# Performance work log

Hardware: AMD Instinct MI355X
Metric: run time of the kernel (lower is better)

## Reference

```python
import jax, jax.numpy as jnp
import numpy as np


def setup_inputs() -> dict:
    key = jax.random.key(0)
    ks = jax.random.split(key, 6)
    B, L, C = 32, 336, 512
    t = L // 2 + 1  # 169 rfft frequencies; four_l must equal t
    s = 1.0 / np.sqrt(C)
    return {
        "x": jax.random.normal(ks[0], (B, L, C), jnp.float32),
        "Wr": jax.random.normal(ks[1], (t, C, C), jnp.float32) * s,  # real part of complex Linear weights [t, out, in]
        "Wi": jax.random.normal(ks[2], (t, C, C), jnp.float32) * s,  # imag part
        "br": jax.random.normal(ks[3], (t, C), jnp.float32) * s,
        "bi": jax.random.normal(ks[4], (t, C), jnp.float32) * s,
        "weights": jax.random.normal(ks[5], (t,), jnp.float32),
    }


def reference(x, Wr, Wi, br, bi, weights):
    # x: [B, L, C] real. rfft along time with ortho norm -> [B, t, C] complex.
    B, L, C = x.shape
    t = Wr.shape[0]
    n = 2 * (t - 1)  # torch irfft default output length (== L, L even)
    xf = jnp.fft.rfft(x, axis=1, norm='ortho')  # [B, t, C] complex64

    # Per-frequency complex linear: y[b,i,o] = sum_c xf[b,i,c] * W[i,o,c] + b[i,o].
    # This fuses the original repeat + eye-mask + python loop into one batched GEMM.
    W = Wr + 1j * Wi
    b = br + 1j * bi
    y = jnp.einsum('bic,ioc->bio', xf, W) + b[None]  # [B, t, C]

    # The original builds fre[b,i,:,c] as a spectrum that is one-hot at frequency i
    # (value y[b,i,c]) and irffts along the frequency axis (ortho norm). For a one-hot
    # spectrum: irfft(onehot_i * y)[l] = scale_i * Re(y * exp(2*pi*j*i*l/n)) / sqrt(n),
    # with scale_i = 2 except at DC (i=0) and Nyquist (i=t-1) where it is 1
    # (imag parts of DC/Nyquist bins are discarded by C2R, matching torch).
    # Finally ConcatenationWithLearnableCoefficient sums over i with softmax weights,
    # so we fold softmax(weights) * scale_i / sqrt(n) into one coefficient per i.
    i_idx = jnp.arange(t)
    scale = jnp.where((i_idx == 0) | (i_idx == t - 1), 1.0, 2.0).astype(jnp.float32)
    w = jax.nn.softmax(weights)
    coef = w * scale / jnp.sqrt(jnp.float32(n))  # [t]

    l_idx = jnp.arange(n)
    theta = (2.0 * jnp.pi / n) * (i_idx[:, None] * l_idx[None, :]).astype(jnp.float32)  # [t, n]
    cos_m, sin_m = jnp.cos(theta), jnp.sin(theta)

    yr = y.real * coef[None, :, None]
    yi = y.imag * coef[None, :, None]
    # Re(y * e^{j theta}) = yr*cos - yi*sin ; sum over frequencies i -> [B, n, C]
    out = jnp.einsum('bic,il->blc', yr, cos_m) - jnp.einsum('bic,il->blc', yi, sin_m)
    return out
```

## Files before the change

kernel.cpp:

```cpp
#include <hip/hip_runtime.h>
#include <math.h>

typedef short   s16x8  __attribute__((ext_vector_type(8)));
typedef __bf16  bf16x8 __attribute__((ext_vector_type(8)));
typedef float   f32x4  __attribute__((ext_vector_type(4)));

#define T_FREQ 169
#define NN     336
#define CCH    512
#define BB     32
#define TP     176
#define LP     352
#define KP     192
#define QK     128

static constexpr size_t OFF_COEF = 0;
static constexpr size_t OFF_FC   = 1024;
static constexpr size_t OFF_FS   = OFF_FC + 124928;
static constexpr size_t OFF_CCOS = OFF_FS + 124928;
static constexpr size_t OFF_CSIN = OFF_CCOS + 130048;
static constexpr size_t OFF_XT   = OFF_CSIN + 130048;
static constexpr size_t OFF_XR   = OFF_XT + (size_t)BB*CCH*LP*2;
static constexpr size_t OFF_XI   = OFF_XR + (size_t)TP*BB*CCH*2;
static constexpr size_t OFF_YR   = OFF_XI + (size_t)TP*BB*CCH*2;
static constexpr size_t OFF_YI   = OFF_YR + (size_t)BB*KP*CCH*2;

__device__ __forceinline__ unsigned short f2bf(float f){
  return __builtin_bit_cast(unsigned short, (__bf16)f);
}

__device__ __forceinline__ bf16x8 cvt8v(f32x4 lo, f32x4 hi){
  bf16x8 r;
  r[0]=(__bf16)lo[0]; r[1]=(__bf16)lo[1]; r[2]=(__bf16)lo[2]; r[3]=(__bf16)lo[3];
  r[4]=(__bf16)hi[0]; r[5]=(__bf16)hi[1]; r[6]=(__bf16)hi[2]; r[7]=(__bf16)hi[3];
  return r;
}

__device__ __forceinline__ f32x4 mfma16(bf16x8 a, bf16x8 b, f32x4 c){
  return __builtin_amdgcn_mfma_f32_16x16x32_bf16(a, b, c, 0, 0, 0);
}

typedef __attribute__((address_space(3))) unsigned lds_u32;
typedef __attribute__((address_space(1))) const unsigned g_u32;
__device__ __forceinline__ void gll16(const void* g, void* l){
  __builtin_amdgcn_global_load_lds((g_u32*)g, (lds_u32*)l, 16, 0, 0);
}

__global__ __launch_bounds__(256) void prep_tables(const float* __restrict__ wts, char* ws){
  float* coef = (float*)(ws + OFF_COEF);
  unsigned short* Fc  = (unsigned short*)(ws + OFF_FC);
  unsigned short* Fs  = (unsigned short*)(ws + OFF_FS);
  unsigned short* Cc  = (unsigned short*)(ws + OFF_CCOS);
  unsigned short* Cs  = (unsigned short*)(ws + OFF_CSIN);
  const float PI2_N = 6.283185307179586f / (float)NN;
  const float inv_sqrt_n = 0.05455447255899809f;

  if (blockIdx.x == 0){
    __shared__ float red[256];
    int tid = threadIdx.x;
    float v = (tid < T_FREQ) ? wts[tid] : -1e30f;
    red[tid] = v; __syncthreads();
    for (int s = 128; s > 0; s >>= 1){ if (tid < s) red[tid] = fmaxf(red[tid], red[tid+s]); __syncthreads(); }
    float mx = red[0]; __syncthreads();
    float e = (tid < T_FREQ) ? expf(v - mx) : 0.f;
    red[tid] = e; __syncthreads();
    for (int s = 128; s > 0; s >>= 1){ if (tid < s) red[tid] += red[tid+s]; __syncthreads(); }
    float ssum = red[0];
    if (tid < T_FREQ){
      float sc = (tid == 0 || tid == T_FREQ-1) ? 1.f : 2.f;
      coef[tid] = (e / ssum) * sc * inv_sqrt_n;
    }
    return;
  }
  int gid = (blockIdx.x - 1) * 256 + threadIdx.x;
  int stride = (gridDim.x - 1) * 256;
  for (int e = gid; e < TP*LP; e += stride){
    int i = e / LP, l = e % LP;
    float c = 0.f, s = 0.f;
    if (l < NN){
      int m = (i * l) % NN;
      float sv, cv; sincosf(PI2_N * (float)m, &sv, &cv);
      c = cv * inv_sqrt_n; s = -sv * inv_sqrt_n;
    }
    Fc[e] = f2bf(c); Fs[e] = f2bf(s);
  }
  for (int e = gid; e < NN*KP; e += stride){
    int l = e / KP, i = e % KP;
    float c = 0.f, s = 0.f;
    if (i < T_FREQ){
      int m = (i * l) % NN;
      float sv, cv; sincosf(PI2_N * (float)m, &sv, &cv);
      c = cv; s = -sv;
    }
    Cc[e] = f2bf(c); Cs[e] = f2bf(s);
  }
}

__global__ __launch_bounds__(256) void transpose_x(const float* __restrict__ x, char* ws){
  unsigned short* xt = (unsigned short*)(ws + OFF_XT);
  __shared__ float tile[32][33];
  int bid = blockIdx.x;
  int b  = bid / (11*16);
  int rm = bid % (11*16);
  int lt = rm / 16, ct = rm % 16;
  int tx = threadIdx.x & 31, ty = threadIdx.x >> 5;
  #pragma unroll
  for (int k = 0; k < 4; ++k){
    int l = lt*32 + ty + k*8;
    int c = ct*32 + tx;
    float v = (l < NN) ? x[((size_t)b*NN + l)*CCH + c] : 0.f;
    tile[ty + k*8][tx] = v;
  }
  __syncthreads();
  #pragma unroll
  for (int k = 0; k < 4; ++k){
    int crow = ct*32 + ty + k*8;
    int lcol = lt*32 + tx;
    xt[((size_t)b*CCH + crow)*LP + lcol] = f2bf(tile[tx][ty + k*8]);
  }
}

__global__ __launch_bounds__(256) void stage_rfft(char* ws){
  const unsigned short* xt = (const unsigned short*)(ws + OFF_XT);
  const unsigned short* Fc = (const unsigned short*)(ws + OFF_FC);
  const unsigned short* Fs = (const unsigned short*)(ws + OFF_FS);
  unsigned short* xr = (unsigned short*)(ws + OFF_XR);
  unsigned short* xi = (unsigned short*)(ws + OFF_XI);

  int bid = blockIdx.x;
  int b  = bid >> 4;
  int rm = bid & 15;
  int c0 = (rm & 7) * 64;
  int mh = rm >> 3;
  int mbase = mh * 5;
  int tid = threadIdx.x, lane = tid & 63, wv = tid >> 6;
  int kg = lane >> 4, ln = lane & 15;
  int c = c0 + wv*16 + ln;

  f32x4 aR[6], aI[6];
  #pragma unroll
  for (int m = 0; m < 6; ++m){ aR[m] = (f32x4){0,0,0,0}; aI[m] = (f32x4){0,0,0,0}; }

  const unsigned short* xrow = xt + ((size_t)b*CCH + c)*LP;
  for (int kk = 0; kk < 11; ++kk){
    int ko = kk*32 + kg*8;
    bf16x8 bx = *(const bf16x8*)(xrow + ko);
    #pragma unroll
    for (int m = 0; m < 6; ++m){
      bf16x8 fc = *(const bf16x8*)(Fc + (size_t)((mbase+m)*16 + ln)*LP + ko);
      bf16x8 fs = *(const bf16x8*)(Fs + (size_t)((mbase+m)*16 + ln)*LP + ko);
      aR[m] = mfma16(fc, bx, aR[m]);
      aI[m] = mfma16(fs, bx, aI[m]);
    }
  }
  int rbase = kg*4;
  #pragma unroll
  for (int m = 0; m < 6; ++m){
    #pragma unroll
    for (int r = 0; r < 4; ++r){
      int i = (mbase+m)*16 + rbase + r;
      size_t off = ((size_t)i*BB + b)*CCH + c;
      xr[off] = f2bf(aR[m][r]);
      xi[off] = f2bf(aI[m][r]);
    }
  }
}

#define WAIT_BAR(N) \
  asm volatile("s_waitcnt vmcnt(" #N ")" ::: "memory"); \
  __builtin_amdgcn_s_barrier(); \
  __builtin_amdgcn_sched_barrier(0)

#define COMPUTE_CHUNK(C) do{ \
  const float* wrr = &sW[C][0][ln][0]; \
  const float* wir = &sW[C][1][ln][0]; \
  _Pragma("unroll") \
  for (int kkl = 0; kkl < 4; ++kkl){ \
    int q0 = ((kkl*8 + kg*2 + 0) ^ ln7) << 2; \
    int q1 = ((kkl*8 + kg*2 + 1) ^ ln7) << 2; \
    f32x4 w0 = *(const f32x4*)(wrr + q0); \
    f32x4 w1 = *(const f32x4*)(wrr + q1); \
    f32x4 v0 = *(const f32x4*)(wir + q0); \
    f32x4 v1 = *(const f32x4*)(wir + q1); \
    bf16x8 wr8 = cvt8v(w0, w1); \
    bf16x8 wi8 = cvt8v(v0, v1); \
    bf16x8 nwi = __builtin_bit_cast(bf16x8, (s16x8)(__builtin_bit_cast(s16x8, wi8) ^ (short)0x8000)); \
    bf16x8 b1 = part ? wi8 : wr8; \
    bf16x8 b2 = part ? wr8 : nwi; \
    acc = mfma16(__builtin_bit_cast(bf16x8, xA[(C)*4 + kkl]), b1, acc); \
    acc = mfma16(__builtin_bit_cast(bf16x8, xB[(C)*4 + kkl]), b2, acc); \
  } \
}while(0)

__global__ __launch_bounds__(256, 2) void stage_cgemm(const float* __restrict__ Wr, const float* __restrict__ Wi,
                                                      const float* __restrict__ br, const float* __restrict__ bi,
                                                      char* ws){
  const unsigned short* xr = (const unsigned short*)(ws + OFF_XR);
  const unsigned short* xi = (const unsigned short*)(ws + OFF_XI);
  const float* coef = (const float*)(ws + OFF_COEF);
  unsigned short* yr = (unsigned short*)(ws + OFF_YR);
  unsigned short* yi = (unsigned short*)(ws + OFF_YI);

  __shared__ float sW[4][2][16][QK];

  int bid = blockIdx.x;
  int i  = bid >> 5;
  int ot = bid & 31;
  int tid = threadIdx.x, lane = tid & 63, wv = tid >> 6;
  int kg = lane >> 4, ln = lane & 15, ln7 = ln & 7;
  int mb = wv & 1, part = wv >> 1;

  const unsigned short* xa = xr + (size_t)(i*BB + mb*16 + ln)*CCH;
  const unsigned short* xb = xi + (size_t)(i*BB + mb*16 + ln)*CCH;
  f32x4 xA[16], xB[16];
  #pragma unroll
  for (int kk = 0; kk < 16; ++kk){
    int ko = kk*32 + kg*8;
    xA[kk] = *(const f32x4*)(xa + ko);
    xB[kk] = *(const f32x4*)(xb + ko);
  }
  #pragma unroll
  for (int kk = 0; kk < 16; ++kk){
    asm volatile("" : "+v"(xA[kk]), "+v"(xB[kk]));
  }
  __builtin_amdgcn_sched_barrier(0);

  {
    const float* wbase = (wv >> 1) ? Wi : Wr;
    const float* gW = wbase + ((size_t)i*CCH + ot*16)*CCH;
    int rl = lane >> 5, g = lane & 31;
    #pragma unroll
    for (int c = 0; c < 4; ++c){
      #pragma unroll
      for (int j = 0; j < 4; ++j){
        int rb = (wv & 1)*8 + j*2;
        int r  = rb + rl;
        int G  = g ^ (r & 7);
        gll16(gW + (size_t)r*CCH + c*QK + G*4, &sW[c][wv>>1][rb][0]);
      }
      __builtin_amdgcn_sched_barrier(0);
    }
  }

  f32x4 acc = (f32x4){0,0,0,0};

  WAIT_BAR(12); COMPUTE_CHUNK(0);
  WAIT_BAR(8);  COMPUTE_CHUNK(1);
  WAIT_BAR(4);  COMPUTE_CHUNK(2);
  WAIT_BAR(0);  COMPUTE_CHUNK(3);

  int o = ot*16 + ln;
  float cf = coef[i];
  float bias = (part ? bi : br)[(size_t)i*CCH + o];
  unsigned short* yp = part ? yi : yr;
  #pragma unroll
  for (int r = 0; r < 4; ++r){
    int bb = mb*16 + kg*4 + r;
    yp[((size_t)bb*KP + i)*CCH + o] = f2bf((acc[r] + bias) * cf);
  }
}

__global__ __launch_bounds__(256) void stage_irfft(const char* ws_c, float* __restrict__ out){
  const char* ws = ws_c;
  const unsigned short* Cc = (const unsigned short*)(ws + OFF_CCOS);
  const unsigned short* Cs = (const unsigned short*)(ws + OFF_CSIN);
  const unsigned short* yr = (const unsigned short*)(ws + OFF_YR);
  const unsigned short* yi = (const unsigned short*)(ws + OFF_YI);

  __shared__ unsigned short lr[64][40];
  __shared__ unsigned short li[64][40];

  int bid = blockIdx.x;
  int b  = bid >> 4;
  int rm = bid & 15;
  int c0 = (rm & 7) * 64;
  int mh = rm >> 3;
  int mbase = mh * 10;
  int tid = threadIdx.x, lane = tid & 63, wv = tid >> 6;
  int kg = lane >> 4, ln = lane & 15;

  f32x4 acc[11];
  #pragma unroll
  for (int m = 0; m < 11; ++m) acc[m] = (f32x4){0,0,0,0};

  for (int kk = 0; kk < 6; ++kk){
    if (kk) __syncthreads();
    #pragma unroll
    for (int q = 0; q < 8; ++q){
      int idx = q*256 + tid;
      int ir = idx >> 6, cc = idx & 63;
      int i = kk*32 + ir;
      unsigned short vr = 0, vi = 0;
      if (i < T_FREQ){
        size_t off = ((size_t)b*KP + i)*CCH + c0 + cc;
        vr = yr[off]; vi = yi[off];
      }
      lr[cc][ir] = vr;
      li[cc][ir] = vi;
    }
    __syncthreads();
    int ko = kk*32 + kg*8;
    bf16x8 blr = *(const bf16x8*)(&lr[wv*16 + ln][kg*8]);
    bf16x8 bli = *(const bf16x8*)(&li[wv*16 + ln][kg*8]);
    #pragma unroll
    for (int m = 0; m < 11; ++m){
      bf16x8 ac = *(const bf16x8*)(Cc + (size_t)((mbase+m)*16 + ln)*KP + ko);
      bf16x8 as = *(const bf16x8*)(Cs + (size_t)((mbase+m)*16 + ln)*KP + ko);
      acc[m] = mfma16(ac, blr, acc[m]);
      acc[m] = mfma16(as, bli, acc[m]);
    }
  }

  int cdst = c0 + wv*16 + ln;
  #pragma unroll
  for (int m = 0; m < 11; ++m){
    #pragma unroll
    for (int r = 0; r < 4; ++r){
      int l = (mbase+m)*16 + kg*4 + r;
      out[((size_t)b*NN + l)*CCH + cdst] = acc[m][r];
    }
  }
}

extern "C" void kernel_launch(void* const* d_in, const int* in_sizes, int n_in,
                              void* d_out, int out_size, void* d_ws, size_t ws_size,
                              hipStream_t stream){
  const float* x   = (const float*)d_in[0];
  const float* Wr  = (const float*)d_in[1];
  const float* Wi  = (const float*)d_in[2];
  const float* br  = (const float*)d_in[3];
  const float* bi  = (const float*)d_in[4];
  const float* wts = (const float*)d_in[5];
  char* ws = (char*)d_ws;

  prep_tables<<<257, 256, 0, stream>>>(wts, ws);
  transpose_x<<<32*11*16, 256, 0, stream>>>(x, ws);
  stage_rfft<<<512, 256, 0, stream>>>(ws);
  stage_cgemm<<<T_FREQ*32, 256, 0, stream>>>(Wr, Wi, br, bi, ws);
  stage_irfft<<<512, 256, 0, stream>>>(ws, (float*)d_out);
}
```

Measured before the change: 203.9 us.

## Pre-convert complex weights to bf16 in MFMA layout before the frequency GEMM

Adds a conversion kernel that reads the fp32 real and imaginary weights and writes them to workspace as bf16, pre-swizzled into the MFMA operand layout. A new GEMM kernel then loads those bf16 fragments directly, with no LDS staging, and runs at higher occupancy. The fallback kernel now reloads x fragments from memory inside the loop instead of keeping them in registers. The conversion runs on every call, so total weight traffic becomes an fp32 read plus a bf16 write plus a bf16 read, which is more than the single fp32 read it replaces. The new path needs a large workspace and runs only when ws_size is big enough.

```diff
diff --git a/kernel.cpp b/kernel.cpp
--- a/kernel.cpp
+++ b/kernel.cpp
@@ -24,9 +24,19 @@
 static constexpr size_t OFF_XI   = OFF_XR + (size_t)TP*BB*CCH*2;
 static constexpr size_t OFF_YR   = OFF_XI + (size_t)TP*BB*CCH*2;
 static constexpr size_t OFF_YI   = OFF_YR + (size_t)BB*KP*CCH*2;
+static constexpr size_t OFF_WB   = OFF_YI + (size_t)BB*KP*CCH*2;
+static constexpr size_t WB_BYTES = (size_t)T_FREQ*2*CCH*CCH*2;
+static constexpr size_t WS_NEED  = OFF_WB + WB_BYTES;
 
 __device__ __forceinline__ unsigned short f2bf(float f){
   return __builtin_bit_cast(unsigned short, (__bf16)f);
+}
+
+__device__ __forceinline__ bf16x8 cvt8(float4 lo, float4 hi){
+  bf16x8 r;
+  r[0]=(__bf16)lo.x; r[1]=(__bf16)lo.y; r[2]=(__bf16)lo.z; r[3]=(__bf16)lo.w;
+  r[4]=(__bf16)hi.x; r[5]=(__bf16)hi.y; r[6]=(__bf16)hi.z; r[7]=(__bf16)hi.w;
+  return r;
 }
 
 __device__ __forceinline__ bf16x8 cvt8v(f32x4 lo, f32x4 hi){
@@ -163,6 +173,71 @@
       xr[off] = f2bf(aR[m][r]);
       xi[off] = f2bf(aI[m][r]);
     }
+  }
+}
+
+__global__ __launch_bounds__(256) void conv_w(const float* __restrict__ Wr, const float* __restrict__ Wi, char* ws){
+  unsigned short* wb = (unsigned short*)(ws + OFF_WB);
+  const size_t total = (size_t)T_FREQ*2*CCH*64;
+  size_t stride = (size_t)gridDim.x * blockDim.x;
+  for (size_t g = (size_t)blockIdx.x*blockDim.x + threadIdx.x; g < total; g += stride){
+    unsigned k8   = (unsigned)(g & 63);
+    unsigned o    = (unsigned)((g >> 6) & 511);
+    unsigned pi   = (unsigned)(g >> 15);
+    unsigned part = pi & 1;
+    unsigned i    = pi >> 1;
+    const float* src = (part ? Wi : Wr) + ((size_t)i*CCH + o)*CCH + k8*8;
+    float4 lo = *(const float4*)(src);
+    float4 hi = *(const float4*)(src + 4);
+    size_t dst = ((((size_t)pi*32 + (o>>4))*16 + (k8>>2))*64 + ((k8&3)*16 + (o&15)))*8;
+    *(bf16x8*)(wb + dst) = cvt8(lo, hi);
+  }
+}
+
+__global__ __launch_bounds__(256, 6) void cgemm_bf(const float* __restrict__ br, const float* __restrict__ bi,
+                                                   char* ws){
+  const unsigned short* xr = (const unsigned short*)(ws + OFF_XR);
+  const unsigned short* xi = (const unsigned short*)(ws + OFF_XI);
+  const unsigned short* wb = (const unsigned short*)(ws + OFF_WB);
+  const float* coef = (const float*)(ws + OFF_COEF);
+  unsigned short* yr = (unsigned short*)(ws + OFF_YR);
+  unsigned short* yi = (unsigned short*)(ws + OFF_YI);
+
+  int bid = blockIdx.x;
+  int i  = bid >> 5;
+  int ot = bid & 31;
+  int tid = threadIdx.x, lane = tid & 63, wv = tid >> 6;
+  int kg = lane >> 4, ln = lane & 15;
+  int mb = wv & 1, part = wv >> 1;
+
+  const unsigned short* xa = xr + (size_t)(i*BB + mb*16 + ln)*CCH;
+  const unsigned short* xb = xi + (size_t)(i*BB + mb*16 + ln)*CCH;
+  const unsigned short* wrp = wb + ((((size_t)(i*2+0)*32 + ot)*16)*64 + lane)*8;
+  const unsigned short* wip = wb + ((((size_t)(i*2+1)*32 + ot)*16)*64 + lane)*8;
+
+  f32x4 acc = (f32x4){0,0,0,0};
+  #pragma unroll
+  for (int kk = 0; kk < 16; ++kk){
+    int ko = kk*32 + kg*8;
+    bf16x8 ar  = *(const bf16x8*)(xa + ko);
+    bf16x8 ai  = *(const bf16x8*)(xb + ko);
+    bf16x8 wr8 = *(const bf16x8*)(wrp + (size_t)kk*512);
+    bf16x8 wi8 = *(const bf16x8*)(wip + (size_t)kk*512);
+    bf16x8 nwi = __builtin_bit_cast(bf16x8, (s16x8)(__builtin_bit_cast(s16x8, wi8) ^ (short)0x8000));
+    bf16x8 b1 = part ? wi8 : wr8;
+    bf16x8 b2 = part ? wr8 : nwi;
+    acc = mfma16(ar, b1, acc);
+    acc = mfma16(ai, b2, acc);
+  }
+
+  int o = ot*16 + ln;
+  float cf = coef[i];
+  float bias = (part ? bi : br)[(size_t)i*CCH + o];
+  unsigned short* yp = part ? yi : yr;
+  #pragma unroll
+  for (int r = 0; r < 4; ++r){
+    int bb = mb*16 + kg*4 + r;
+    yp[((size_t)bb*KP + i)*CCH + o] = f2bf((acc[r] + bias) * cf);
   }
 }
 
@@ -187,8 +262,11 @@
     bf16x8 nwi = __builtin_bit_cast(bf16x8, (s16x8)(__builtin_bit_cast(s16x8, wi8) ^ (short)0x8000)); \
     bf16x8 b1 = part ? wi8 : wr8; \
     bf16x8 b2 = part ? wr8 : nwi; \
-    acc = mfma16(__builtin_bit_cast(bf16x8, xA[(C)*4 + kkl]), b1, acc); \
-    acc = mfma16(__builtin_bit_cast(bf16x8, xB[(C)*4 + kkl]), b2, acc); \
+    int ko = (C)*QK + kkl*32 + kg*8; \
+    bf16x8 ar = *(const bf16x8*)(xa + ko); \
+    bf16x8 ai = *(const bf16x8*)(xb + ko); \
+    acc = mfma16(ar, b1, acc); \
+    acc = mfma16(ai, b2, acc); \
   } \
 }while(0)
 
@@ -212,18 +290,6 @@
 
   const unsigned short* xa = xr + (size_t)(i*BB + mb*16 + ln)*CCH;
   const unsigned short* xb = xi + (size_t)(i*BB + mb*16 + ln)*CCH;
-  f32x4 xA[16], xB[16];
-  #pragma unroll
-  for (int kk = 0; kk < 16; ++kk){
-    int ko = kk*32 + kg*8;
-    xA[kk] = *(const f32x4*)(xa + ko);
-    xB[kk] = *(const f32x4*)(xb + ko);
-  }
-  #pragma unroll
-  for (int kk = 0; kk < 16; ++kk){
-    asm volatile("" : "+v"(xA[kk]), "+v"(xB[kk]));
-  }
-  __builtin_amdgcn_sched_barrier(0);
 
   {
     const float* wbase = (wv >> 1) ? Wi : Wr;
@@ -333,9 +399,18 @@
   const float* wts = (const float*)d_in[5];
   char* ws = (char*)d_ws;
 
+  const bool two_pass = (ws_size >= WS_NEED);
+
+  if (two_pass){
+    conv_w<<<2048, 256, 0, stream>>>(Wr, Wi, ws);
+  }
   prep_tables<<<257, 256, 0, stream>>>(wts, ws);
   transpose_x<<<32*11*16, 256, 0, stream>>>(x, ws);
   stage_rfft<<<512, 256, 0, stream>>>(ws);
-  stage_cgemm<<<T_FREQ*32, 256, 0, stream>>>(Wr, Wi, br, bi, ws);
+  if (two_pass){
+    cgemm_bf<<<T_FREQ*32, 256, 0, stream>>>(br, bi, ws);
+  } else {
+    stage_cgemm<<<T_FREQ*32, 256, 0, stream>>>(Wr, Wi, br, bi, ws);
+  }
   stage_irfft<<<512, 256, 0, stream>>>(ws, (float*)d_out);
 }
```

Measured after the change: 364.6 us. 1.79x slower.
